# Performance work log

Measured on AMD Instinct MI355X. Metric: run time of the kernel, lower is better.

Reference implementation:

```python
import jax, jax.numpy as jnp
import numpy as np

EPS = 1e-5


def _layernorm(x, w, b):
    mu = jnp.mean(x, axis=-1, keepdims=True)
    xc = x - mu
    var = jnp.mean(xc * xc, axis=-1, keepdims=True)
    return xc * jax.lax.rsqrt(var + EPS) * w + b


def _s5_ssm(u, lam_re, lam_im, log_step, B_re, B_im, C_re, C_im, Dvec):
    # u: [B,L,D]; diagonal complex SSM with ZOH discretization + associative scan
    Lam = lam_re + 1j * lam_im                      # [P]
    step = jnp.exp(log_step)                        # [P]
    Abar = jnp.exp(Lam * step)                      # [P]
    Bbar = ((Abar - 1.0) / Lam)[:, None] * (B_re + 1j * B_im)  # [P,D]
    Bu = jnp.einsum('bld,pd->blp', u.astype(jnp.complex64), Bbar)  # [B,L,P]
    A_el = jnp.broadcast_to(Abar, Bu.shape)

    def binop(e1, e2):
        a1, b1 = e1
        a2, b2 = e2
        return a1 * a2, a2 * b1 + b2

    _, xs = jax.lax.associative_scan(binop, (A_el, Bu), axis=1)  # [B,L,P] complex
    y = jnp.einsum('blp,dp->bld', xs, C_re + 1j * C_im).real + Dvec * u
    return y


def _s5_block(x, an_w, an_b, lam_re, lam_im, log_step, B_re, B_im, C_re, C_im,
              Dvec, fn_w, fn_b, Wenc, Wdec):
    fx = _layernorm(x, an_w, an_b)
    s = _s5_ssm(fx, lam_re, lam_im, log_step, B_re, B_im, C_re, C_im, Dvec)
    z = jax.nn.gelu(s, approximate=False) + fx
    fy = _layernorm(z, fn_w, fn_b)
    h = fy @ Wenc.T                                  # [B,L,2D]
    a, g = jnp.split(h, 2, axis=-1)                  # GEGLU
    return (a * jax.nn.gelu(g, approximate=False)) @ Wdec.T + fy


def setup_inputs() -> dict:
    D = 1048   # d_model
    P = 1048   # state_dim
    NL = 3
    Bsz, L = 4, 4096
    key = jax.random.key(0)
    ks = jax.random.split(key, 20)
    f32 = jnp.float32
    inp = {}
    inp['x'] = jax.random.normal(ks[0], (Bsz, L, 1), f32)
    inp['enc_w'] = jax.random.normal(ks[1], (D, 1), f32)
    inp['enc_b'] = jnp.zeros((D,), f32)
    inp['norm_w'] = jnp.ones((NL, D), f32)
    inp['norm_b'] = jnp.zeros((NL, D), f32)
    inp['attn_norm_w'] = jnp.ones((NL, D), f32)
    inp['attn_norm_b'] = jnp.zeros((NL, D), f32)
    inp['ff_norm_w'] = jnp.ones((NL, D), f32)
    inp['ff_norm_b'] = jnp.zeros((NL, D), f32)
    # stable diagonal dynamics: Re(Lambda) < 0
    inp['lam_re'] = -0.5 * jax.random.uniform(ks[2], (NL, P), f32) - 0.05
    inp['lam_im'] = np.float32(np.pi) * jax.random.normal(ks[3], (NL, P), f32)
    lo, hi = np.float32(np.log(1e-3)), np.float32(np.log(1e-1))
    inp['log_step'] = lo + (hi - lo) * jax.random.uniform(ks[4], (NL, P), f32)
    sB = np.float32(1.0 / np.sqrt(D))
    sC = np.float32(1.0 / np.sqrt(P))
    inp['B_re'] = sB * jax.random.normal(ks[5], (NL, P, D), f32)
    inp['B_im'] = sB * jax.random.normal(ks[6], (NL, P, D), f32)
    inp['C_re'] = sC * jax.random.normal(ks[7], (NL, D, P), f32)
    inp['C_im'] = sC * jax.random.normal(ks[8], (NL, D, P), f32)
    inp['Dvec'] = jax.random.normal(ks[9], (NL, D), f32)
    sW = np.float32(1.0 / np.sqrt(D))
    inp['Wenc'] = sW * jax.random.normal(ks[10], (NL, 2 * D, D), f32)
    inp['Wdec'] = sW * jax.random.normal(ks[11], (NL, D, D), f32)
    inp['head_w'] = sW * jax.random.normal(ks[12], (1, D), f32)
    inp['head_b'] = jnp.zeros((1,), f32)
    return inp


def reference(x, enc_w, enc_b, norm_w, norm_b, attn_norm_w, attn_norm_b,
              ff_norm_w, ff_norm_b, lam_re, lam_im, log_step, B_re, B_im,
              C_re, C_im, Dvec, Wenc, Wdec, head_w, head_b):
    h = x @ enc_w.T + enc_b                          # [B,L,D]
    n_layers = norm_w.shape[0]
    for i in range(n_layers):                        # small fixed loop over layers
        z = _layernorm(h, norm_w[i], norm_b[i])      # prenorm
        z = _s5_block(z, attn_norm_w[i], attn_norm_b[i], lam_re[i], lam_im[i],
                      log_step[i], B_re[i], B_im[i], C_re[i], C_im[i],
                      Dvec[i], ff_norm_w[i], ff_norm_b[i], Wenc[i], Wdec[i])
        h = h + z                                    # residual (dropout = identity in eval)
    pooled = jnp.mean(h, axis=1)                     # [B,D]
    y = (pooled @ head_w.T + head_b).squeeze(-1)     # [B]
    return y
```

## Files before the change

### kernel.cpp

```cpp
#include <hip/hip_runtime.h>
#include <hip/hip_bf16.h>
#include <cstddef>

typedef __hip_bfloat16 bf16;

#define D_MODEL 1048
#define P_DIM   1048
#define NLAYER  3
#define BSZ     4
#define LSEQ    4096
#define BL      (BSZ*LSEQ)
#define BLD     ((size_t)BL*D_MODEL)
#define KP      1056
#define NP      1152
#define BLA     ((size_t)BL*KP)
#define NPKP    ((size_t)NP*KP)

#define NC      64
#define CL      (LSEQ/NC)
#define NSCAN   (BSZ*NC*P_DIM)
#define P2      (P_DIM/2)
#define NSCAN2  (BSZ*NC*P2)

typedef __attribute__((ext_vector_type(8))) short short8;
typedef __attribute__((ext_vector_type(4))) float f32x4;

#define TM 128
#define TN 128
#define TK 32
#define TILE_SH (TM*TK)
#define NGEMM   ((BL/TM)*(NP/TN))

__device__ __forceinline__ float gelu_f(float x) {
    return 0.5f * x * (1.f + erff(x * 0.70710678118654752f));
}

__device__ __forceinline__ void tile_coords(int id, int& m0, int& n0) {
    int xcd  = id & 7;
    int slot = id >> 3;
    int xg   = slot / 9;
    int j    = slot - xg*9;
    m0 = (xg*8 + xcd) * TM;
    n0 = j * TN;
}

__device__ __forceinline__ void stage_tile(
    const bf16* __restrict__ src, int row0, int k0, short* lds, int tid)
{
#pragma unroll
    for (int c = 0; c < 2; ++c) {
        int chunk = tid + 256*c;
        int r = chunk >> 2;
        int col = (chunk & 3) * 8;
        __builtin_amdgcn_global_load_lds(
            (const __attribute__((address_space(1))) void*)(src + (size_t)(row0 + r)*KP + k0 + col),
            (__attribute__((address_space(3))) void*)(lds + chunk*8), 16, 0, 0);
    }
}

__device__ __forceinline__ void mfma_step1(
    const short* As, const short* Ws, f32x4 (&acc)[4][4],
    int wm, int wn, int row_in, int quad)
{
    short8 a[4], b[4];
#pragma unroll
    for (int i = 0; i < 4; ++i) {
        a[i] = *(const short8*)&As[(wm + i*16 + row_in)*TK + quad*8];
        b[i] = *(const short8*)&Ws[(wn + i*16 + row_in)*TK + quad*8];
    }
#pragma unroll
    for (int i = 0; i < 4; ++i)
#pragma unroll
        for (int j = 0; j < 4; ++j)
            acc[i][j] = __builtin_amdgcn_mfma_f32_16x16x32_bf16(a[i], b[j], acc[i][j], 0, 0, 0);
}

__device__ __forceinline__ void mfma_step2(
    const short* As, const short* W0s, const short* W1s,
    f32x4 (&acc0)[4][4], f32x4 (&acc1)[4][4],
    int wm, int wn, int row_in, int quad)
{
    short8 a[4], b0[4], b1[4];
#pragma unroll
    for (int i = 0; i < 4; ++i) {
        a[i]  = *(const short8*)&As [(wm + i*16 + row_in)*TK + quad*8];
        b0[i] = *(const short8*)&W0s[(wn + i*16 + row_in)*TK + quad*8];
        b1[i] = *(const short8*)&W1s[(wn + i*16 + row_in)*TK + quad*8];
    }
#pragma unroll
    for (int i = 0; i < 4; ++i)
#pragma unroll
        for (int j = 0; j < 4; ++j) {
            acc0[i][j] = __builtin_amdgcn_mfma_f32_16x16x32_bf16(a[i], b0[j], acc0[i][j], 0, 0, 0);
            acc1[i][j] = __builtin_amdgcn_mfma_f32_16x16x32_bf16(a[i], b1[j], acc1[i][j], 0, 0, 0);
        }
}

template <int MODE>
__global__ __launch_bounds__(256, 2) void gemm2o_k(
    const bf16* __restrict__ A, const bf16* __restrict__ W0,
    const bf16* __restrict__ W1,
    bf16* __restrict__ O0, bf16* __restrict__ O1, int N)
{
    __shared__ short As[2*TILE_SH];
    __shared__ short W0s[2*TILE_SH];
    __shared__ short W1s[2*TILE_SH];
    const int tid  = threadIdx.x;
    int m0, n0;
    tile_coords(blockIdx.x, m0, n0);
    const int wave = tid >> 6, lane = tid & 63;
    const int wm = (wave >> 1) * 64, wn = (wave & 1) * 64;
    const int row_in = lane & 15, quad = lane >> 4;

    f32x4 acc0[4][4] = {};
    f32x4 acc1[4][4] = {};

    for (int kt = 0; kt < 16; ++kt) {
        const int k0 = kt*64;
        stage_tile(A,  m0, k0,      As,            tid);
        stage_tile(A,  m0, k0 + 32, As + TILE_SH,  tid);
        stage_tile(W0, n0, k0,      W0s,           tid);
        stage_tile(W0, n0, k0 + 32, W0s + TILE_SH, tid);
        stage_tile(W1, n0, k0,      W1s,           tid);
        stage_tile(W1, n0, k0 + 32, W1s + TILE_SH, tid);
        __syncthreads();
        mfma_step2(As,           W0s,           W1s,           acc0, acc1, wm, wn, row_in, quad);
        mfma_step2(As + TILE_SH, W0s + TILE_SH, W1s + TILE_SH, acc0, acc1, wm, wn, row_in, quad);
        __syncthreads();
    }
    stage_tile(A,  m0, 1024, As,  tid);
    stage_tile(W0, n0, 1024, W0s, tid);
    stage_tile(W1, n0, 1024, W1s, tid);
    __syncthreads();
    mfma_step2(As, W0s, W1s, acc0, acc1, wm, wn, row_in, quad);

#pragma unroll
    for (int i = 0; i < 4; ++i) {
#pragma unroll
        for (int j = 0; j < 4; ++j) {
            int n = n0 + wn + j*16 + row_in;
#pragma unroll
            for (int r = 0; r < 4; ++r) {
                int m = m0 + wm + i*16 + quad*4 + r;
                size_t o = (size_t)m*KP + n;
                if (MODE == 0) {
                    if (n < N)        { O0[o] = __float2bfloat16(acc0[i][j][r]);
                                        O1[o] = __float2bfloat16(acc1[i][j][r]); }
                    else if (n < KP)  { O0[o] = __float2bfloat16(0.f);
                                        O1[o] = __float2bfloat16(0.f); }
                } else {
                    if (n < N)        O0[o] = __float2bfloat16(acc0[i][j][r] * gelu_f(acc1[i][j][r]));
                    else if (n < KP)  O0[o] = __float2bfloat16(0.f);
                }
            }
        }
    }
}

__global__ __launch_bounds__(256) void gemmC_k(
    const bf16* __restrict__ A0, const bf16* __restrict__ W0,
    const bf16* __restrict__ A1, const bf16* __restrict__ W1,
    const bf16* __restrict__ fx, const float* __restrict__ dv,
    bf16* __restrict__ O, int N)
{
    __shared__ short As[2*TILE_SH];
    __shared__ short Ws[2*TILE_SH];
    const int tid  = threadIdx.x;
    int m0, n0;
    tile_coords(blockIdx.x, m0, n0);
    const int wave = tid >> 6, lane = tid & 63;
    const int wm = (wave >> 1) * 64, wn = (wave & 1) * 64;
    const int row_in = lane & 15, quad = lane >> 4;

    f32x4 acc[4][4] = {};

    for (int pair = 0; pair < 2; ++pair) {
        const bf16* A = pair ? A1 : A0;
        const bf16* W = pair ? W1 : W0;
        for (int kt = 0; kt < 16; ++kt) {
            const int k0 = kt*64;
            stage_tile(A, m0, k0,      As,           tid);
            stage_tile(A, m0, k0 + 32, As + TILE_SH, tid);
            stage_tile(W, n0, k0,      Ws,           tid);
            stage_tile(W, n0, k0 + 32, Ws + TILE_SH, tid);
            __syncthreads();
            mfma_step1(As,           Ws,           acc, wm, wn, row_in, quad);
            mfma_step1(As + TILE_SH, Ws + TILE_SH, acc, wm, wn, row_in, quad);
            __syncthreads();
        }
        stage_tile(A, m0, 1024, As, tid);
        stage_tile(W, n0, 1024, Ws, tid);
        __syncthreads();
        mfma_step1(As, Ws, acc, wm, wn, row_in, quad);
        __syncthreads();
    }

#pragma unroll
    for (int i = 0; i < 4; ++i) {
#pragma unroll
        for (int j = 0; j < 4; ++j) {
            int n = n0 + wn + j*16 + row_in;
#pragma unroll
            for (int r = 0; r < 4; ++r) {
                int m = m0 + wm + i*16 + quad*4 + r;
                size_t o = (size_t)m*KP + n;
                if (n < N) {
                    float f = __bfloat162float(fx[o]);
                    float t = acc[i][j][r] + dv[n]*f;
                    O[o] = __float2bfloat16(gelu_f(t) + f);
                } else if (n < KP) {
                    O[o] = __float2bfloat16(0.f);
                }
            }
        }
    }
}

__global__ __launch_bounds__(256) void gemmD_k(
    const bf16* __restrict__ A, const bf16* __restrict__ W,
    const bf16* __restrict__ fy, float* __restrict__ h, int N)
{
    __shared__ short As[2*TILE_SH];
    __shared__ short Ws[2*TILE_SH];
    const int tid  = threadIdx.x;
    int m0, n0;
    tile_coords(blockIdx.x, m0, n0);
    const int wave = tid >> 6, lane = tid & 63;
    const int wm = (wave >> 1) * 64, wn = (wave & 1) * 64;
    const int row_in = lane & 15, quad = lane >> 4;

    f32x4 acc[4][4] = {};

    for (int kt = 0; kt < 16; ++kt) {
        const int k0 = kt*64;
        stage_tile(A, m0, k0,      As,           tid);
        stage_tile(A, m0, k0 + 32, As + TILE_SH, tid);
        stage_tile(W, n0, k0,      Ws,           tid);
        stage_tile(W, n0, k0 + 32, Ws + TILE_SH, tid);
        __syncthreads();
        mfma_step1(As,           Ws,           acc, wm, wn, row_in, quad);
        mfma_step1(As + TILE_SH, Ws + TILE_SH, acc, wm, wn, row_in, quad);
        __syncthreads();
    }
    stage_tile(A, m0, 1024, As, tid);
    stage_tile(W, n0, 1024, Ws, tid);
    __syncthreads();
    mfma_step1(As, Ws, acc, wm, wn, row_in, quad);

#pragma unroll
    for (int i = 0; i < 4; ++i) {
#pragma unroll
        for (int j = 0; j < 4; ++j) {
            int n = n0 + wn + j*16 + row_in;
            if (n >= N) continue;
#pragma unroll
            for (int r = 0; r < 4; ++r) {
                int m = m0 + wm + i*16 + quad*4 + r;
                float f = __bfloat162float(fy[(size_t)m*KP + n]);
                h[(size_t)m*D_MODEL + n] += acc[i][j][r] + f;
            }
        }
    }
}

__global__ __launch_bounds__(256) void convw5_k(
    const float* __restrict__ s0, const float* __restrict__ s1,
    const float* __restrict__ s2, const float* __restrict__ s3,
    const float* __restrict__ s4, bf16* __restrict__ dst)
{
    size_t i = (size_t)blockIdx.x*256 + threadIdx.x;
    if (i >= NPKP) return;
    int z = blockIdx.z;
    const float* src = (z == 0) ? s0 : (z == 1) ? s1 : (z == 2) ? s2 : (z == 3) ? s3 : s4;
    float scale = (z == 1) ? -1.f : 1.f;
    int n = (int)(i / KP), k = (int)(i - (size_t)n*KP);
    float v = (n < D_MODEL && k < D_MODEL) ? scale*src[(size_t)n*D_MODEL + k] : 0.f;
    dst[(size_t)z*NPKP + i] = __float2bfloat16(v);
}

__device__ __forceinline__ float2 block_reduce2(float a, float b) {
    __syncthreads();
    for (int off = 32; off; off >>= 1) {
        a += __shfl_down(a, off, 64);
        b += __shfl_down(b, off, 64);
    }
    __shared__ float sa[4], sb[4];
    int lane = threadIdx.x & 63, wv = threadIdx.x >> 6;
    if (lane == 0) { sa[wv] = a; sb[wv] = b; }
    __syncthreads();
    if (threadIdx.x == 0) {
        sa[0] = sa[0]+sa[1]+sa[2]+sa[3];
        sb[0] = sb[0]+sb[1]+sb[2]+sb[3];
    }
    __syncthreads();
    return make_float2(sa[0], sb[0]);
}

template <int ENC>
__global__ __launch_bounds__(256) void ln2x_k(
    const float* __restrict__ xin,
    const float* __restrict__ ew, const float* __restrict__ eb,
    float* __restrict__ hbuf,
    const float* __restrict__ w1, const float* __restrict__ bb1,
    const float* __restrict__ w2, const float* __restrict__ bb2,
    bf16* __restrict__ y)
{
    const size_t row = blockIdx.x;
    float v[5];
    float s = 0.f, ss = 0.f;
    int i = 0;
    if (ENC) {
        float xv = xin[row];
        float* hr = hbuf + row * D_MODEL;
        for (int d = threadIdx.x; d < KP; d += 256, ++i) {
            float t = 0.f;
            if (d < D_MODEL) { t = xv*ew[d] + eb[d]; hr[d] = t; }
            v[i] = t; s += t; ss += t*t;
        }
    } else {
        const float* xr = hbuf + row * D_MODEL;
        for (int d = threadIdx.x; d < KP; d += 256, ++i) {
            float t = (d < D_MODEL) ? xr[d] : 0.f;
            v[i] = t; s += t; ss += t*t;
        }
    }
    float2 r = block_reduce2(s, ss);
    float mu  = r.x * (1.f/D_MODEL);
    float var = r.y * (1.f/D_MODEL) - mu*mu;
    float inv = rsqrtf(var + 1e-5f);
    s = 0.f; ss = 0.f; i = 0;
    for (int d = threadIdx.x; d < KP; d += 256, ++i) {
        float z = (d < D_MODEL) ? (v[i]-mu)*inv*w1[d] + bb1[d] : 0.f;
        v[i] = z; s += z; ss += z*z;
    }
    r = block_reduce2(s, ss);
    mu  = r.x * (1.f/D_MODEL);
    var = r.y * (1.f/D_MODEL) - mu*mu;
    inv = rsqrtf(var + 1e-5f);
    bf16* yr = y + row * KP;
    i = 0;
    for (int d = threadIdx.x; d < KP; d += 256, ++i) {
        float o = (d < D_MODEL) ? (v[i]-mu)*inv*w2[d] + bb2[d] : 0.f;
        yr[d] = __float2bfloat16(o);
    }
}

__global__ __launch_bounds__(256) void ln_k(
    const bf16* __restrict__ x, const float* __restrict__ w,
    const float* __restrict__ b, bf16* __restrict__ y)
{
    const size_t row = blockIdx.x;
    const bf16* xr = x + row * KP;
    float v[5];
    float s = 0.f, ss = 0.f;
    int i = 0;
    for (int d = threadIdx.x; d < KP; d += 256, ++i) {
        float t = (d < D_MODEL) ? __bfloat162float(xr[d]) : 0.f;
        v[i] = t; s += t; ss += t*t;
    }
    float2 r = block_reduce2(s, ss);
    float mu  = r.x * (1.f/D_MODEL);
    float var = r.y * (1.f/D_MODEL) - mu*mu;
    float inv = rsqrtf(var + 1e-5f);
    bf16* yr = y + row * KP;
    i = 0;
    for (int d = threadIdx.x; d < KP; d += 256, ++i) {
        float o = (d < D_MODEL) ? (v[i]-mu)*inv*w[d] + b[d] : 0.f;
        yr[d] = __float2bfloat16(o);
    }
}

__global__ __launch_bounds__(256) void prep_k(
    const float* __restrict__ lam_re, const float* __restrict__ lam_im,
    const float* __restrict__ log_step,
    const float* __restrict__ B_re, const float* __restrict__ B_im,
    bf16* __restrict__ bbar_re, bf16* __restrict__ bbar_im,
    float* __restrict__ abar)
{
    size_t idx = (size_t)blockIdx.x*256 + threadIdx.x;
    if (idx >= NPKP) return;
    int p = (int)(idx / KP);
    int d = (int)(idx - (size_t)p*KP);
    if (p >= P_DIM || d >= D_MODEL) {
        bbar_re[idx] = __float2bfloat16(0.f);
        bbar_im[idx] = __float2bfloat16(0.f);
        return;
    }
    float lr = lam_re[p], li = lam_im[p];
    float st = expf(log_step[p]);
    float er = expf(lr*st);
    float ar = er * cosf(li*st);
    float ai = er * sinf(li*st);
    if (d == 0) { abar[p] = ar; abar[P_DIM + p] = ai; }
    float den = lr*lr + li*li;
    float xr = ar - 1.f, xi = ai;
    float cr = (xr*lr + xi*li) / den;
    float ci = (xi*lr - xr*li) / den;
    float br = B_re[(size_t)p*D_MODEL + d], bi = B_im[(size_t)p*D_MODEL + d];
    bbar_re[idx] = __float2bfloat16(cr*br - ci*bi);
    bbar_im[idx] = __float2bfloat16(cr*bi + ci*br);
}

__device__ __forceinline__ float2 bf2f(unsigned int u) {
    unsigned int lo = u << 16, hi = u & 0xffff0000u;
    float2 r;
    r.x = __uint_as_float(lo);
    r.y = __uint_as_float(hi);
    return r;
}
__device__ __forceinline__ unsigned int f2bf2(float a, float b) {
    bf16 ba = __float2bfloat16(a), bb = __float2bfloat16(b);
    unsigned short ua = *(unsigned short*)&ba, ub = *(unsigned short*)&bb;
    return (unsigned int)ua | ((unsigned int)ub << 16);
}

__global__ __launch_bounds__(256) void scan_partial_k(
    const unsigned int* __restrict__ ur, const unsigned int* __restrict__ ui,
    const float* __restrict__ abar,
    float* __restrict__ sum_re, float* __restrict__ sum_im)
{
    int idx = blockIdx.x*256 + threadIdx.x;
    if (idx >= NSCAN2) return;
    int p2 = idx % P2;
    int rest = idx / P2;
    int c = rest % NC, b = rest / NC;
    int p = 2*p2;
    float ar0 = abar[p],   ai0 = abar[P_DIM + p];
    float ar1 = abar[p+1], ai1 = abar[P_DIM + p + 1];
    size_t base = (((size_t)b*LSEQ + (size_t)c*CL)*KP + p) >> 1;
    float s0r = 0.f, s0i = 0.f, s1r = 0.f, s1i = 0.f;
    for (int i = 0; i < CL; ++i) {
        size_t o = base + (size_t)i*(KP/2);
        float2 br = bf2f(ur[o]);
        float2 bi = bf2f(ui[o]);
        float n0r = fmaf(ar0, s0r, fmaf(-ai0, s0i, br.x));
        float n0i = fmaf(ar0, s0i, fmaf( ai0, s0r, bi.x));
        float n1r = fmaf(ar1, s1r, fmaf(-ai1, s1i, br.y));
        float n1i = fmaf(ar1, s1i, fmaf( ai1, s1r, bi.y));
        s0r = n0r; s0i = n0i; s1r = n1r; s1i = n1i;
    }
    size_t so = ((size_t)b*NC + c)*P_DIM + p;
    *(float2*)&sum_re[so] = make_float2(s0r, s1r);
    *(float2*)&sum_im[so] = make_float2(s0i, s1i);
}

__global__ __launch_bounds__(256) void scan_carry_k(
    const float* __restrict__ sum_re, const float* __restrict__ sum_im,
    const float* __restrict__ abar,
    float* __restrict__ car_re, float* __restrict__ car_im)
{
    int idx = blockIdx.x*256 + threadIdx.x;
    if (idx >= BSZ*P_DIM) return;
    int p = idx % P_DIM, b = idx / P_DIM;
    float cr = abar[p], ci = abar[P_DIM + p];
#pragma unroll
    for (int s = 0; s < 6; ++s) {
        float nr = cr*cr - ci*ci;
        float ni = 2.f*cr*ci;
        cr = nr; ci = ni;
    }
    float xre = 0.f, xim = 0.f;
    size_t base = (size_t)b*NC*P_DIM + p;
    for (int c = 0; c < NC; ++c) {
        size_t o = base + (size_t)c*P_DIM;
        car_re[o] = xre; car_im[o] = xim;
        float sre = sum_re[o], sim = sum_im[o];
        float nr = fmaf(cr, xre, fmaf(-ci, xim, sre));
        float ni = fmaf(cr, xim, fmaf( ci, xre, sim));
        xre = nr; xim = ni;
    }
}

__global__ __launch_bounds__(256) void scan_apply_k(
    unsigned int* __restrict__ ur, unsigned int* __restrict__ ui,
    const float* __restrict__ abar,
    const float* __restrict__ car_re, const float* __restrict__ car_im)
{
    int idx = blockIdx.x*256 + threadIdx.x;
    if (idx >= NSCAN2) return;
    int p2 = idx % P2;
    int rest = idx / P2;
    int c = rest % NC, b = rest / NC;
    int p = 2*p2;
    float ar0 = abar[p],   ai0 = abar[P_DIM + p];
    float ar1 = abar[p+1], ai1 = abar[P_DIM + p + 1];
    size_t co = ((size_t)b*NC + c)*P_DIM + p;
    float2 c_r = *(const float2*)&car_re[co];
    float2 c_i = *(const float2*)&car_im[co];
    float x0r = c_r.x, x0i = c_i.x, x1r = c_r.y, x1i = c_i.y;
    size_t base = (((size_t)b*LSEQ + (size_t)c*CL)*KP + p) >> 1;
    for (int i = 0; i < CL; ++i) {
        size_t o = base + (size_t)i*(KP/2);
        float2 br = bf2f(ur[o]);
        float2 bi = bf2f(ui[o]);
        float n0r = fmaf(ar0, x0r, fmaf(-ai0, x0i, br.x));
        float n0i = fmaf(ar0, x0i, fmaf( ai0, x0r, bi.x));
        float n1r = fmaf(ar1, x1r, fmaf(-ai1, x1i, br.y));
        float n1i = fmaf(ar1, x1i, fmaf( ai1, x1r, bi.y));
        x0r = n0r; x0i = n0i; x1r = n1r; x1i = n1i;
        ur[o] = f2bf2(x0r, x1r);
        ui[o] = f2bf2(x0i, x1i);
    }
}

__global__ void head_init_k(float* out, const float* hb)
{
    if (threadIdx.x < BSZ) out[threadIdx.x] = hb[0];
}

__global__ __launch_bounds__(256) void head_k(
    const float* __restrict__ h, const float* __restrict__ hw,
    float* __restrict__ out)
{
    int b = blockIdx.x;
    int chunk = blockIdx.y;
    const float* hb = h + ((size_t)b*LSEQ + (size_t)chunk*64)*D_MODEL;
    float s = 0.f;
    for (int l = 0; l < 64; ++l) {
        const float* hr = hb + (size_t)l*D_MODEL;
        for (int d = threadIdx.x; d < D_MODEL; d += 256)
            s += hr[d]*hw[d];
    }
    for (int off = 32; off; off >>= 1) s += __shfl_down(s, off, 64);
    __shared__ float sm[4];
    int lane = threadIdx.x & 63, wv = threadIdx.x >> 6;
    if (lane == 0) sm[wv] = s;
    __syncthreads();
    if (threadIdx.x == 0)
        atomicAdd(out + b, (sm[0]+sm[1]+sm[2]+sm[3]) * (1.f/LSEQ));
}

extern "C" void kernel_launch(void* const* d_in, const int* in_sizes, int n_in,
                              void* d_out, int out_size, void* d_ws, size_t ws_size,
                              hipStream_t stream)
{
    const float* x          = (const float*)d_in[0];
    const float* enc_w      = (const float*)d_in[1];
    const float* enc_b      = (const float*)d_in[2];
    const float* norm_w     = (const float*)d_in[3];
    const float* norm_b     = (const float*)d_in[4];
    const float* attn_w     = (const float*)d_in[5];
    const float* attn_b     = (const float*)d_in[6];
    const float* ff_w       = (const float*)d_in[7];
    const float* ff_b       = (const float*)d_in[8];
    const float* lam_re     = (const float*)d_in[9];
    const float* lam_im     = (const float*)d_in[10];
    const float* log_step   = (const float*)d_in[11];
    const float* B_re       = (const float*)d_in[12];
    const float* B_im       = (const float*)d_in[13];
    const float* C_re       = (const float*)d_in[14];
    const float* C_im       = (const float*)d_in[15];
    const float* Dvec       = (const float*)d_in[16];
    const float* Wenc       = (const float*)d_in[17];
    const float* Wdec       = (const float*)d_in[18];
    const float* head_w     = (const float*)d_in[19];
    const float* head_b     = (const float*)d_in[20];
    float* out = (float*)d_out;

    float* h    = (float*)d_ws;
    bf16*  b1   = (bf16*)(h + BLD);
    bf16*  b2   = b1 + BLA;
    bf16*  b3   = b2 + BLA;
    bf16*  b4   = b3 + BLA;
    bf16*  wbr  = b4 + BLA;
    bf16*  wbi  = wbr + NPKP;
    bf16*  w5   = wbi + NPKP;
    bf16*  wcr  = w5;
    bf16*  wci  = w5 + NPKP;
    bf16*  wea  = w5 + 2*NPKP;
    bf16*  weg  = w5 + 3*NPKP;
    bf16*  wd   = w5 + 4*NPKP;
    float* abar = (float*)(w5 + 5*NPKP);
    float* sum_re = abar + 2*P_DIM;
    float* sum_im = sum_re + NSCAN;
    float* car_re = sum_im + NSCAN;
    float* car_im = car_re + NSCAN;

    const int CV   = (int)((NPKP + 255)/256);
    const int SC_G = (NSCAN2 + 255)/256;
    const size_t pd = (size_t)P_DIM*D_MODEL;

    for (int i = 0; i < NLAYER; ++i) {
        prep_k<<<CV, 256, 0, stream>>>(
            lam_re + i*P_DIM, lam_im + i*P_DIM, log_step + i*P_DIM,
            B_re + i*pd, B_im + i*pd, wbr, wbi, abar);
        const float* WencA = Wenc + (size_t)i*2*pd;
        const float* WencG = WencA + pd;
        convw5_k<<<dim3(CV,1,5), 256, 0, stream>>>(
            C_re + i*pd, C_im + i*pd, WencA, WencG, Wdec + i*pd, w5);

        if (i == 0)
            ln2x_k<1><<<BL, 256, 0, stream>>>(x, enc_w, enc_b, h,
                norm_w + i*D_MODEL, norm_b + i*D_MODEL,
                attn_w + i*D_MODEL, attn_b + i*D_MODEL, b2);
        else
            ln2x_k<0><<<BL, 256, 0, stream>>>(nullptr, nullptr, nullptr, h,
                norm_w + i*D_MODEL, norm_b + i*D_MODEL,
                attn_w + i*D_MODEL, attn_b + i*D_MODEL, b2);

        gemm2o_k<0><<<NGEMM, 256, 0, stream>>>(b2, wbr, wbi, b1, b3, P_DIM);

        scan_partial_k<<<SC_G, 256, 0, stream>>>((unsigned int*)b1, (unsigned int*)b3,
                                                 abar, sum_re, sum_im);
        scan_carry_k<<<(BSZ*P_DIM + 255)/256, 256, 0, stream>>>(sum_re, sum_im, abar, car_re, car_im);
        scan_apply_k<<<SC_G, 256, 0, stream>>>((unsigned int*)b1, (unsigned int*)b3,
                                               abar, car_re, car_im);

        gemmC_k<<<NGEMM, 256, 0, stream>>>(b1, wcr, b3, wci, b2, Dvec + i*D_MODEL, b4, D_MODEL);

        ln_k<<<BL, 256, 0, stream>>>(b4, ff_w + i*D_MODEL, ff_b + i*D_MODEL, b1);

        gemm2o_k<1><<<NGEMM, 256, 0, stream>>>(b1, wea, weg, b2, nullptr, D_MODEL);

        gemmD_k<<<NGEMM, 256, 0, stream>>>(b2, wd, b1, h, D_MODEL);
    }

    head_init_k<<<1, 64, 0, stream>>>(out, head_b);
    head_k<<<dim3(BSZ, 64), 256, 0, stream>>>(h, head_w, out);
}
```

Measured before the change: 2.107 ms.

## Double-buffer GEMM K-loop with async LDS prefetch and XOR-swizzled LDS layout

The three bf16 MFMA GEMM kernels switch from a load-all-then-compute loop with two full syncthreads per 64-wide K chunk to a two-stage ping-pong pipeline. The load for step s+2 is issued right after step s's compute, and partial vmcnt waits let global->LDS loads overlap MFMA work. The LDS column chunk is XOR-swizzled by row on both the store and read side to reduce bank conflicts on the short8 reads. gemmC/gemmD also get launch_bounds(256,2). The manual vmcnt counts must match the number of outstanding loads exactly, which is fragile if the compiler reorders or splits loads.

```diff
diff --git a/kernel.cpp b/kernel.cpp
--- a/kernel.cpp
+++ b/kernel.cpp
@@ -30,6 +30,7 @@
 #define TK 32
 #define TILE_SH (TM*TK)
 #define NGEMM   ((BL/TM)*(NP/TN))
+#define KSTEPS  (KP/TK)
 
 __device__ __forceinline__ float gelu_f(float x) {
     return 0.5f * x * (1.f + erff(x * 0.70710678118654752f));
@@ -51,7 +52,7 @@
     for (int c = 0; c < 2; ++c) {
         int chunk = tid + 256*c;
         int r = chunk >> 2;
-        int col = (chunk & 3) * 8;
+        int col = ((chunk ^ (r >> 1)) & 3) * 8;
         __builtin_amdgcn_global_load_lds(
             (const __attribute__((address_space(1))) void*)(src + (size_t)(row0 + r)*KP + k0 + col),
             (__attribute__((address_space(3))) void*)(lds + chunk*8), 16, 0, 0);
@@ -60,13 +61,13 @@
 
 __device__ __forceinline__ void mfma_step1(
     const short* As, const short* Ws, f32x4 (&acc)[4][4],
-    int wm, int wn, int row_in, int quad)
+    int wm, int wn, int row_in, int qs)
 {
     short8 a[4], b[4];
 #pragma unroll
     for (int i = 0; i < 4; ++i) {
-        a[i] = *(const short8*)&As[(wm + i*16 + row_in)*TK + quad*8];
-        b[i] = *(const short8*)&Ws[(wn + i*16 + row_in)*TK + quad*8];
+        a[i] = *(const short8*)&As[(wm + i*16 + row_in)*TK + qs];
+        b[i] = *(const short8*)&Ws[(wn + i*16 + row_in)*TK + qs];
     }
 #pragma unroll
     for (int i = 0; i < 4; ++i)
@@ -78,14 +79,14 @@
 __device__ __forceinline__ void mfma_step2(
     const short* As, const short* W0s, const short* W1s,
     f32x4 (&acc0)[4][4], f32x4 (&acc1)[4][4],
-    int wm, int wn, int row_in, int quad)
+    int wm, int wn, int row_in, int qs)
 {
     short8 a[4], b0[4], b1[4];
 #pragma unroll
     for (int i = 0; i < 4; ++i) {
-        a[i]  = *(const short8*)&As [(wm + i*16 + row_in)*TK + quad*8];
-        b0[i] = *(const short8*)&W0s[(wn + i*16 + row_in)*TK + quad*8];
-        b1[i] = *(const short8*)&W1s[(wn + i*16 + row_in)*TK + quad*8];
+        a[i]  = *(const short8*)&As [(wm + i*16 + row_in)*TK + qs];
+        b0[i] = *(const short8*)&W0s[(wn + i*16 + row_in)*TK + qs];
+        b1[i] = *(const short8*)&W1s[(wn + i*16 + row_in)*TK + qs];
     }
 #pragma unroll
     for (int i = 0; i < 4; ++i)
@@ -102,38 +103,45 @@
     const bf16* __restrict__ W1,
     bf16* __restrict__ O0, bf16* __restrict__ O1, int N)
 {
-    __shared__ short As[2*TILE_SH];
-    __shared__ short W0s[2*TILE_SH];
-    __shared__ short W1s[2*TILE_SH];
+    __shared__ __align__(16) short As[2][TILE_SH];
+    __shared__ __align__(16) short W0s[2][TILE_SH];
+    __shared__ __align__(16) short W1s[2][TILE_SH];
     const int tid  = threadIdx.x;
     int m0, n0;
     tile_coords(blockIdx.x, m0, n0);
     const int wave = tid >> 6, lane = tid & 63;
     const int wm = (wave >> 1) * 64, wn = (wave & 1) * 64;
-    const int row_in = lane & 15, quad = lane >> 4;
+    const int row_in = lane & 15;
+    const int qs = (((lane >> 4) ^ (lane >> 1)) & 3) * 8;
 
     f32x4 acc0[4][4] = {};
     f32x4 acc1[4][4] = {};
 
-    for (int kt = 0; kt < 16; ++kt) {
-        const int k0 = kt*64;
-        stage_tile(A,  m0, k0,      As,            tid);
-        stage_tile(A,  m0, k0 + 32, As + TILE_SH,  tid);
-        stage_tile(W0, n0, k0,      W0s,           tid);
-        stage_tile(W0, n0, k0 + 32, W0s + TILE_SH, tid);
-        stage_tile(W1, n0, k0,      W1s,           tid);
-        stage_tile(W1, n0, k0 + 32, W1s + TILE_SH, tid);
-        __syncthreads();
-        mfma_step2(As,           W0s,           W1s,           acc0, acc1, wm, wn, row_in, quad);
-        mfma_step2(As + TILE_SH, W0s + TILE_SH, W1s + TILE_SH, acc0, acc1, wm, wn, row_in, quad);
-        __syncthreads();
-    }
-    stage_tile(A,  m0, 1024, As,  tid);
-    stage_tile(W0, n0, 1024, W0s, tid);
-    stage_tile(W1, n0, 1024, W1s, tid);
-    __syncthreads();
-    mfma_step2(As, W0s, W1s, acc0, acc1, wm, wn, row_in, quad);
-
+    stage_tile(A,  m0, 0,  As[0],  tid);
+    stage_tile(W0, n0, 0,  W0s[0], tid);
+    stage_tile(W1, n0, 0,  W1s[0], tid);
+    stage_tile(A,  m0, 32, As[1],  tid);
+    stage_tile(W0, n0, 32, W0s[1], tid);
+    stage_tile(W1, n0, 32, W1s[1], tid);
+
+    for (int s = 0; s < KSTEPS - 1; ++s) {
+        asm volatile("s_waitcnt vmcnt(6)" ::: "memory");
+        __builtin_amdgcn_s_barrier();
+        mfma_step2(As[s & 1], W0s[s & 1], W1s[s & 1], acc0, acc1, wm, wn, row_in, qs);
+        __builtin_amdgcn_s_barrier();
+        if (s < KSTEPS - 2) {
+            const int k0 = (s + 2) * TK;
+            stage_tile(A,  m0, k0, As[s & 1],  tid);
+            stage_tile(W0, n0, k0, W0s[s & 1], tid);
+            stage_tile(W1, n0, k0, W1s[s & 1], tid);
+        }
+    }
+    asm volatile("s_waitcnt vmcnt(0)" ::: "memory");
+    __builtin_amdgcn_s_barrier();
+    mfma_step2(As[(KSTEPS-1) & 1], W0s[(KSTEPS-1) & 1], W1s[(KSTEPS-1) & 1],
+               acc0, acc1, wm, wn, row_in, qs);
+
+    const int quad = lane >> 4;
 #pragma unroll
     for (int i = 0; i < 4; ++i) {
 #pragma unroll
@@ -157,44 +165,49 @@
     }
 }
 
-__global__ __launch_bounds__(256) void gemmC_k(
+__global__ __launch_bounds__(256, 2) void gemmC_k(
     const bf16* __restrict__ A0, const bf16* __restrict__ W0,
     const bf16* __restrict__ A1, const bf16* __restrict__ W1,
     const bf16* __restrict__ fx, const float* __restrict__ dv,
     bf16* __restrict__ O, int N)
 {
-    __shared__ short As[2*TILE_SH];
-    __shared__ short Ws[2*TILE_SH];
+    __shared__ __align__(16) short As[2][TILE_SH];
+    __shared__ __align__(16) short Ws[2][TILE_SH];
     const int tid  = threadIdx.x;
     int m0, n0;
     tile_coords(blockIdx.x, m0, n0);
     const int wave = tid >> 6, lane = tid & 63;
     const int wm = (wave >> 1) * 64, wn = (wave & 1) * 64;
-    const int row_in = lane & 15, quad = lane >> 4;
+    const int row_in = lane & 15;
+    const int qs = (((lane >> 4) ^ (lane >> 1)) & 3) * 8;
 
     f32x4 acc[4][4] = {};
 
-    for (int pair = 0; pair < 2; ++pair) {
-        const bf16* A = pair ? A1 : A0;
-        const bf16* W = pair ? W1 : W0;
-        for (int kt = 0; kt < 16; ++kt) {
-            const int k0 = kt*64;
-            stage_tile(A, m0, k0,      As,           tid);
-            stage_tile(A, m0, k0 + 32, As + TILE_SH, tid);
-            stage_tile(W, n0, k0,      Ws,           tid);
-            stage_tile(W, n0, k0 + 32, Ws + TILE_SH, tid);
-            __syncthreads();
-            mfma_step1(As,           Ws,           acc, wm, wn, row_in, quad);
-            mfma_step1(As + TILE_SH, Ws + TILE_SH, acc, wm, wn, row_in, quad);
-            __syncthreads();
-        }
-        stage_tile(A, m0, 1024, As, tid);
-        stage_tile(W, n0, 1024, Ws, tid);
-        __syncthreads();
-        mfma_step1(As, Ws, acc, wm, wn, row_in, quad);
-        __syncthreads();
-    }
-
+    const int NST = 2*KSTEPS;
+    stage_tile(A0, m0, 0,  As[0], tid);
+    stage_tile(W0, n0, 0,  Ws[0], tid);
+    stage_tile(A0, m0, 32, As[1], tid);
+    stage_tile(W0, n0, 32, Ws[1], tid);
+
+    for (int s = 0; s < NST - 1; ++s) {
+        asm volatile("s_waitcnt vmcnt(4)" ::: "memory");
+        __builtin_amdgcn_s_barrier();
+        mfma_step1(As[s & 1], Ws[s & 1], acc, wm, wn, row_in, qs);
+        __builtin_amdgcn_s_barrier();
+        if (s < NST - 2) {
+            int t = s + 2;
+            const bf16* A = (t >= KSTEPS) ? A1 : A0;
+            const bf16* W = (t >= KSTEPS) ? W1 : W0;
+            int kk = (t >= KSTEPS) ? t - KSTEPS : t;
+            stage_tile(A, m0, kk*TK, As[s & 1], tid);
+            stage_tile(W, n0, kk*TK, Ws[s & 1], tid);
+        }
+    }
+    asm volatile("s_waitcnt vmcnt(0)" ::: "memory");
+    __builtin_amdgcn_s_barrier();
+    mfma_step1(As[(NST-1) & 1], Ws[(NST-1) & 1], acc, wm, wn, row_in, qs);
+
+    const int quad = lane >> 4;
 #pragma unroll
     for (int i = 0; i < 4; ++i) {
 #pragma unroll
@@ -216,37 +229,43 @@
     }
 }
 
-__global__ __launch_bounds__(256) void gemmD_k(
+__global__ __launch_bounds__(256, 2) void gemmD_k(
     const bf16* __restrict__ A, const bf16* __restrict__ W,
     const bf16* __restrict__ fy, float* __restrict__ h, int N)
 {
-    __shared__ short As[2*TILE_SH];
-    __shared__ short Ws[2*TILE_SH];
+    __shared__ __align__(16) short As[2][TILE_SH];
+    __shared__ __align__(16) short Ws[2][TILE_SH];
     const int tid  = threadIdx.x;
     int m0, n0;
     tile_coords(blockIdx.x, m0, n0);
     const int wave = tid >> 6, lane = tid & 63;
     const int wm = (wave >> 1) * 64, wn = (wave & 1) * 64;
-    const int row_in = lane & 15, quad = lane >> 4;
+    const int row_in = lane & 15;
+    const int qs = (((lane >> 4) ^ (lane >> 1)) & 3) * 8;
 
     f32x4 acc[4][4] = {};
 
-    for (int kt = 0; kt < 16; ++kt) {
-        const int k0 = kt*64;
-        stage_tile(A, m0, k0,      As,           tid);
-        stage_tile(A, m0, k0 + 32, As + TILE_SH, tid);
-        stage_tile(W, n0, k0,      Ws,           tid);
-        stage_tile(W, n0, k0 + 32, Ws + TILE_SH, tid);
-        __syncthreads();
-        mfma_step1(As,           Ws,           acc, wm, wn, row_in, quad);
-        mfma_step1(As + TILE_SH, Ws + TILE_SH, acc, wm, wn, row_in, quad);
-        __syncthreads();
-    }
-    stage_tile(A, m0, 1024, As, tid);
-    stage_tile(W, n0, 1024, Ws, tid);
-    __syncthreads();
-    mfma_step1(As, Ws, acc, wm, wn, row_in, quad);
-
+    stage_tile(A, m0, 0,  As[0], tid);
+    stage_tile(W, n0, 0,  Ws[0], tid);
+    stage_tile(A, m0, 32, As[1], tid);
+    stage_tile(W, n0, 32, Ws[1], tid);
+
+    for (int s = 0; s < KSTEPS - 1; ++s) {
+        asm volatile("s_waitcnt vmcnt(4)" ::: "memory");
+        __builtin_amdgcn_s_barrier();
+        mfma_step1(As[s & 1], Ws[s & 1], acc, wm, wn, row_in, qs);
+        __builtin_amdgcn_s_barrier();
+        if (s < KSTEPS - 2) {
+            const int k0 = (s + 2) * TK;
+            stage_tile(A, m0, k0, As[s & 1], tid);
+            stage_tile(W, n0, k0, Ws[s & 1], tid);
+        }
+    }
+    asm volatile("s_waitcnt vmcnt(0)" ::: "memory");
+    __builtin_amdgcn_s_barrier();
+    mfma_step1(As[(KSTEPS-1) & 1], Ws[(KSTEPS-1) & 1], acc, wm, wn, row_in, qs);
+
+    const int quad = lane >> 4;
 #pragma unroll
     for (int i = 0; i < 4; ++i) {
 #pragma unroll
```

New measurement: 2.020 ms. 4.1% less time.
